# Optimization experiments

Hardware: AMD Instinct MI355X
Metric: run time of the kernel (lower is better)

## Reference

```python
import jax, jax.numpy as jnp
import numpy as np

N = 20000      # nodes
E = 640000     # edges (before self loops)
IN = 256       # in_channels == out_channels (forced by classifier size 4*in)
H1, C1 = 8, 16   # conv1: heads=8, out=16 -> concat 128
H2, C2 = 1, 256  # conv2: heads=1, out=out_channels
B = 4096       # article pairs
NEG_SLOPE = 0.2  # PyG GATv2Conv default negative_slope


def setup_inputs() -> dict:
    key = jax.random.key(0)
    ks = jax.random.split(key, 24)
    s = 0.05
    inp = {
        "gnn_x": jax.random.normal(ks[0], (N, IN), jnp.float32),
        "vanilla_x": jax.random.normal(ks[1], (N, IN), jnp.float32),
        "edge_src": jax.random.randint(ks[2], (E,), 0, N, jnp.int32),
        "edge_dst": jax.random.randint(ks[3], (E,), 0, N, jnp.int32),
        "a1_idx": jax.random.randint(ks[4], (B,), 0, N, jnp.int64),
        "a2_idx": jax.random.randint(ks[5], (B,), 0, N, jnp.int64),
        # conv1 params (lin_l, lin_r, att, bias)
        "Wl1": jax.random.normal(ks[6], (IN, H1 * C1), jnp.float32) * s,
        "bl1": jnp.zeros((H1 * C1,), jnp.float32),
        "Wr1": jax.random.normal(ks[7], (IN, H1 * C1), jnp.float32) * s,
        "br1": jnp.zeros((H1 * C1,), jnp.float32),
        "att1": jax.random.normal(ks[8], (H1, C1), jnp.float32) * s,
        "bias1": jnp.zeros((H1 * C1,), jnp.float32),
        # conv2 params
        "Wl2": jax.random.normal(ks[9], (H1 * C1, H2 * C2), jnp.float32) * s,
        "bl2": jnp.zeros((H2 * C2,), jnp.float32),
        "Wr2": jax.random.normal(ks[10], (H1 * C1, H2 * C2), jnp.float32) * s,
        "br2": jnp.zeros((H2 * C2,), jnp.float32),
        "att2": jax.random.normal(ks[11], (H2, C2), jnp.float32) * s,
        "bias2": jnp.zeros((H2 * C2,), jnp.float32),
        # classifier
        "Wc": jax.random.normal(ks[12], (4 * IN, 1), jnp.float32) * s,
        "bc": jnp.zeros((1,), jnp.float32),
    }
    return inp


def _gatv2_layer(x, src, dst, Wl, bl, Wr, br, att, bias):
    """GATv2Conv: x_l = lin_l(x)[src], x_r = lin_r(x)[dst];
    e = att . leaky_relu(x_l + x_r); segment softmax over dst; scatter-add x_l*alpha."""
    n = x.shape[0]
    h, c = att.shape
    xl = (x @ Wl + bl).reshape(n, h, c)
    xr = (x @ Wr + br).reshape(n, h, c)
    # per-edge attention logits [E, H]
    e = jnp.einsum('ehc,hc->eh', jax.nn.leaky_relu(xl[src] + xr[dst], NEG_SLOPE), att)
    # segment softmax over destination nodes (self loops guarantee non-empty segments)
    emax = jax.ops.segment_max(e, dst, num_segments=n)
    ex = jnp.exp(e - emax[dst])
    denom = jax.ops.segment_sum(ex, dst, num_segments=n)
    alpha = ex / denom[dst]                      # [E, H]
    out = jax.ops.segment_sum(alpha[:, :, None] * xl[src], dst, num_segments=n)  # [N,H,C]
    return out.reshape(n, h * c) + bias          # concat=True (heads=1 identical)


def reference(gnn_x, vanilla_x, Wl1, bl1, Wr1, br1, att1, bias1,
              Wl2, bl2, Wr2, br2, att2, bias2, Wc, bc,
              edge_src, edge_dst, a1_idx, a2_idx):
    n = gnn_x.shape[0]
    loops = jnp.arange(n, dtype=edge_src.dtype)
    src = jnp.concatenate([edge_src, loops])     # PyG add_self_loops=True
    dst = jnp.concatenate([edge_dst, loops])
    x = _gatv2_layer(gnn_x, src, dst, Wl1, bl1, Wr1, br1, att1, bias1)
    x = jax.nn.relu(x)
    x = _gatv2_layer(x, src, dst, Wl2, bl2, Wr2, br2, att2, bias2)
    combined = jnp.concatenate(
        [vanilla_x[a1_idx], vanilla_x[a2_idx], x[a1_idx], x[a2_idx]], axis=1)  # [B, 4*IN]
    logits = combined @ Wc + bc                  # [B, 1]
    return logits
```

## Files before the change

kernel.cpp:

```cpp
#include <hip/hip_runtime.h>
#include <math.h>

#define N_NODES 20000
#define M_PAD   20032
#define E_EDGES 640000
#define ET (E_EDGES + N_NODES)
#define IN_CH 256
#define D1 128
#define D2 256
#define BPAIRS 4096
#define NEG 0.2f
#define LOG2E 1.4426950408889634f

#define ZC_BLOCKS    20
#define WT_BLOCKS    32
#define XCONV_BLOCKS (M_PAD * IN_CH / 4 / 4 / 256)
#define RANK_BLOCKS  ((ET + 255) / 256)

#define G1X (M_PAD / 64)
#define G1Y (D1 / 64)
#define G1_BLOCKS (G1X * G1Y)
#define SCAT_BLOCKS ((ET + 255) / 256)

#if __has_builtin(__builtin_amdgcn_exp2f)
#define EXP2F(x) __builtin_amdgcn_exp2f(x)
#else
#define EXP2F(x) exp2f(x)
#endif

typedef __bf16 bf16x8 __attribute__((ext_vector_type(8)));
typedef float  f32x4  __attribute__((ext_vector_type(4)));
typedef float  f32x2  __attribute__((ext_vector_type(2)));
typedef unsigned short u16x4 __attribute__((ext_vector_type(4)));

__device__ __forceinline__ unsigned short f2b(float f) {
    unsigned int u = __float_as_uint(f);
    unsigned int r = u + 0x7FFFu + ((u >> 16) & 1u);
    return (unsigned short)(r >> 16);
}
__device__ __forceinline__ unsigned char f2f8(float f) {
    return (unsigned char)(__builtin_amdgcn_cvt_pk_fp8_f32(f, f, 0, false) & 0xFF);
}
template <bool HI>
__device__ __forceinline__ f32x2 f8up2(unsigned int u) {
    return __builtin_amdgcn_cvt_pk_f32_fp8((int)u, HI);
}
__device__ __forceinline__ f32x2 up2(unsigned int u) {
    f32x2 r;
    r.x = __uint_as_float(u << 16);
    r.y = __uint_as_float(u & 0xFFFF0000u);
    return r;
}
__device__ __forceinline__ f32x2 lrelu2(f32x2 s) {
    return __builtin_elementwise_max(s, s * NEG);
}
__device__ __forceinline__ float lrelu(float s) { return fmaxf(s, NEG * s); }

__device__ __forceinline__ void unpack8(uint4 u, float* v) {
    v[0] = __uint_as_float(u.x << 16); v[1] = __uint_as_float(u.x & 0xFFFF0000u);
    v[2] = __uint_as_float(u.y << 16); v[3] = __uint_as_float(u.y & 0xFFFF0000u);
    v[4] = __uint_as_float(u.z << 16); v[5] = __uint_as_float(u.z & 0xFFFF0000u);
    v[6] = __uint_as_float(u.w << 16); v[7] = __uint_as_float(u.w & 0xFFFF0000u);
}
__device__ __forceinline__ void unpack8_f8(uint2 u, float* v) {
    f32x2 a = f8up2<false>(u.x), b = f8up2<true>(u.x);
    f32x2 c = f8up2<false>(u.y), d = f8up2<true>(u.y);
    v[0] = a.x; v[1] = a.y; v[2] = b.x; v[3] = b.y;
    v[4] = c.x; v[5] = c.y; v[6] = d.x; v[7] = d.y;
}


__global__ __launch_bounds__(256) void prep_kernel(
        const float* __restrict__ gnn_x,
        const float* __restrict__ Wl1, const float* __restrict__ Wr1,
        const float* __restrict__ Wl2, const float* __restrict__ Wr2,
        unsigned short* __restrict__ xb,
        unsigned short* __restrict__ wt1l, unsigned short* __restrict__ wt1r,
        unsigned short* __restrict__ wt2l, unsigned short* __restrict__ wt2r,
        int* __restrict__ count) {
    __shared__ unsigned short tile[64 * 65];
    int bid = blockIdx.x;
    if (bid < ZC_BLOCKS) {
        int q = bid * 256 + threadIdx.x;
        if (q * 4 < N_NODES) {
            int4 z; z.x = z.y = z.z = z.w = 0;
            ((int4*)count)[q] = z;
        }
    } else if (bid < ZC_BLOCKS + WT_BLOCKS) {
        int t = bid - ZC_BLOCKS;
        int m = t >> 3;
        int tt = t & 7;
        const float* W;
        unsigned short* Wt;
        int K, N;
        if (m == 0)      { W = Wl1; Wt = wt1l; K = IN_CH; N = D1; }
        else if (m == 1) { W = Wr1; Wt = wt1r; K = IN_CH; N = D1; }
        else if (m == 2) { W = Wl2; Wt = wt2l; K = D1; N = D2; }
        else             { W = Wr2; Wt = wt2r; K = D1; N = D2; }
        int ntn = N >> 6;
        int k0 = (tt / ntn) << 6;
        int n0 = (tt % ntn) << 6;
        int c = threadIdx.x & 63;
        int rr = threadIdx.x >> 6;
#pragma unroll
        for (int ch = 0; ch < 16; ch++) {
            int row = rr * 16 + ch;
            tile[row * 65 + c] = f2b(W[(size_t)(k0 + row) * N + n0 + c]);
        }
        __syncthreads();
#pragma unroll
        for (int ch = 0; ch < 16; ch++) {
            int n = rr * 16 + ch;
            Wt[(size_t)(n0 + n) * K + k0 + c] = tile[c * 65 + n];
        }
    } else {
        int tid = (bid - ZC_BLOCKS - WT_BLOCKS) * 256 + threadIdx.x;
        const int NQ = M_PAD * IN_CH / 4;
        int q0 = tid * 4;
#pragma unroll
        for (int j = 0; j < 4; j++) {
            int qi = q0 + j;
            if (qi >= NQ) break;
            int e0 = qi * 4;
            int row = e0 >> 8;
            u16x4 o;
            if (row < N_NODES) {
                f32x4 v = __builtin_nontemporal_load((const f32x4*)(gnn_x + e0));
                o.x = f2b(v.x); o.y = f2b(v.y); o.z = f2b(v.z); o.w = f2b(v.w);
            } else {
                o.x = o.y = o.z = o.w = 0;
            }
            *(u16x4*)(xb + e0) = o;
        }
    }
}


__global__ __launch_bounds__(256) void rank_kernel(
        const int* __restrict__ edge_dst,
        int* __restrict__ count, int* __restrict__ rank) {
    int e = blockIdx.x * 256 + threadIdx.x;
    if (e >= ET) return;
    int dst = (e < E_EDGES) ? edge_dst[e] : (e - E_EDGES);
    rank[e] = atomicAdd(&count[dst], 1);
}


__global__ __launch_bounds__(1024) void scan_kernel(const int* __restrict__ count,
                                                    int* __restrict__ offsets) {
    const int PER = 20;
    int t = threadIdx.x;
    int base = t * PER;
    int local[PER];
    int sum = 0;
#pragma unroll
    for (int i = 0; i < PER; i++) {
        int idx = base + i;
        int v = (idx < N_NODES) ? count[idx] : 0;
        local[i] = sum;
        sum += v;
    }
    int lane = t & 63, wave = t >> 6;
    int s = sum;
#pragma unroll
    for (int off = 1; off < 64; off <<= 1) {
        int x = __shfl_up(s, off);
        if (lane >= off) s += x;
    }
    __shared__ int wsum[16];
    __shared__ int wpre[16];
    if (lane == 63) wsum[wave] = s;
    __syncthreads();
    if (t == 0) {
        int acc = 0;
        for (int w = 0; w < 16; w++) { wpre[w] = acc; acc += wsum[w]; }
        offsets[N_NODES] = acc;
    }
    __syncthreads();
    int thread_excl = wpre[wave] + (s - sum);
#pragma unroll
    for (int i = 0; i < PER; i++) {
        int idx = base + i;
        if (idx < N_NODES) offsets[idx] = thread_excl + local[i];
    }
}


template <int K>
__device__ __forceinline__ void dual_gemm_tile(
        const unsigned short* __restrict__ A,
        const unsigned short* __restrict__ Wtl,
        const unsigned short* __restrict__ Wtr,
        const float* __restrict__ bl, const float* __restrict__ br,
        unsigned char* __restrict__ Yl, unsigned short* __restrict__ Yr,
        int M, int NOUT, int bx, int by) {
    const int NK = K / 32;
    int wave = threadIdx.x >> 6;
    int lane = threadIdx.x & 63;
    int row0 = bx * 64;
    int col0 = (by * 4 + wave) * 16;
    int rsub = lane & 15;
    int koff = (lane >> 4) * 8;

    const unsigned short* ap  = A   + (size_t)(row0 + rsub) * K + koff;
    const unsigned short* bpl = Wtl + (size_t)(col0 + rsub) * K + koff;
    const unsigned short* bpr = Wtr + (size_t)(col0 + rsub) * K + koff;

    bf16x8 bfl[NK], bfr[NK];
#pragma unroll
    for (int kb = 0; kb < NK; kb++) {
        bfl[kb] = *(const bf16x8*)(bpl + kb * 32);
        bfr[kb] = *(const bf16x8*)(bpr + kb * 32);
    }

    f32x4 l0 = {0.f, 0.f, 0.f, 0.f};
    f32x4 l1 = l0, l2 = l0, l3 = l0, r0 = l0, r1 = l0, r2 = l0, r3 = l0;

#pragma unroll
    for (int kb = 0; kb < NK; kb++) {
        int off = kb * 32;
        bf16x8 a0 = *(const bf16x8*)(ap + off);
        bf16x8 a1 = *(const bf16x8*)(ap + 16 * K + off);
        bf16x8 a2 = *(const bf16x8*)(ap + 32 * K + off);
        bf16x8 a3 = *(const bf16x8*)(ap + 48 * K + off);
        l0 = __builtin_amdgcn_mfma_f32_16x16x32_bf16(a0, bfl[kb], l0, 0, 0, 0);
        r0 = __builtin_amdgcn_mfma_f32_16x16x32_bf16(a0, bfr[kb], r0, 0, 0, 0);
        l1 = __builtin_amdgcn_mfma_f32_16x16x32_bf16(a1, bfl[kb], l1, 0, 0, 0);
        r1 = __builtin_amdgcn_mfma_f32_16x16x32_bf16(a1, bfr[kb], r1, 0, 0, 0);
        l2 = __builtin_amdgcn_mfma_f32_16x16x32_bf16(a2, bfl[kb], l2, 0, 0, 0);
        r2 = __builtin_amdgcn_mfma_f32_16x16x32_bf16(a2, bfr[kb], r2, 0, 0, 0);
        l3 = __builtin_amdgcn_mfma_f32_16x16x32_bf16(a3, bfl[kb], l3, 0, 0, 0);
        r3 = __builtin_amdgcn_mfma_f32_16x16x32_bf16(a3, bfr[kb], r3, 0, 0, 0);
    }

    int colg = col0 + rsub;
    float bvl = bl[colg];
    float bvr = br[colg];
    int rbase = row0 + (lane >> 4) * 4;
#pragma unroll
    for (int t = 0; t < 4; t++) {
        f32x4 al = (t == 0) ? l0 : (t == 1) ? l1 : (t == 2) ? l2 : l3;
        f32x4 ar = (t == 0) ? r0 : (t == 1) ? r1 : (t == 2) ? r2 : r3;
#pragma unroll
        for (int r = 0; r < 4; r++) {
            int row = rbase + t * 16 + r;
            if (row < M) {
                Yl[(size_t)row * NOUT + colg] = f2f8(al[r] + bvl);
                Yr[(size_t)row * NOUT + colg] = f2b(ar[r] + bvr);
            }
        }
    }
}


__global__ __launch_bounds__(256) void gemm1_scatter_kernel(
        const unsigned short* __restrict__ A,
        const unsigned short* __restrict__ Wtl,
        const unsigned short* __restrict__ Wtr,
        const float* __restrict__ bl, const float* __restrict__ br,
        unsigned char* __restrict__ Yl, unsigned short* __restrict__ Yr,
        const int* __restrict__ edge_src, const int* __restrict__ edge_dst,
        const int* __restrict__ rank, const int* __restrict__ offsets,
        int* __restrict__ sorted_src) {
    int bid = blockIdx.x;
    if (bid < G1_BLOCKS) {
        dual_gemm_tile<IN_CH>(A, Wtl, Wtr, bl, br, Yl, Yr,
                              N_NODES, D1, bid % G1X, bid / G1X);
    } else {
        int e = (bid - G1_BLOCKS) * 256 + threadIdx.x;
        if (e >= ET) return;
        int dst = (e < E_EDGES) ? edge_dst[e] : (e - E_EDGES);
        int src = (e < E_EDGES) ? edge_src[e] : (e - E_EDGES);
        sorted_src[offsets[dst] + rank[e]] = src;
    }
}


template <int K>
__global__ __launch_bounds__(256) void dual_gemm_w32_kernel(
        const unsigned short* __restrict__ A,
        const unsigned short* __restrict__ Wtl,
        const unsigned short* __restrict__ Wtr,
        const float* __restrict__ bl, const float* __restrict__ br,
        unsigned char* __restrict__ Yl, unsigned short* __restrict__ Yr,
        int M, int NOUT) {
    const int NK = K / 32;
    int wave = threadIdx.x >> 6;
    int lane = threadIdx.x & 63;
    int row0 = blockIdx.x * 64;
    int col0 = blockIdx.y * 128 + wave * 32;
    int rsub = lane & 15;
    int koff = (lane >> 4) * 8;

    const unsigned short* ap = A + (size_t)(row0 + rsub) * K + koff;

    bf16x8 bfl[2][NK], bfr[2][NK];
#pragma unroll
    for (int c = 0; c < 2; c++) {
        const unsigned short* bpl = Wtl + (size_t)(col0 + c * 16 + rsub) * K + koff;
        const unsigned short* bpr = Wtr + (size_t)(col0 + c * 16 + rsub) * K + koff;
#pragma unroll
        for (int kb = 0; kb < NK; kb++) {
            bfl[c][kb] = *(const bf16x8*)(bpl + kb * 32);
            bfr[c][kb] = *(const bf16x8*)(bpr + kb * 32);
        }
    }

    f32x4 accl[2][4], accr[2][4];
#pragma unroll
    for (int c = 0; c < 2; c++)
#pragma unroll
        for (int t = 0; t < 4; t++) {
            accl[c][t] = (f32x4){0.f, 0.f, 0.f, 0.f};
            accr[c][t] = (f32x4){0.f, 0.f, 0.f, 0.f};
        }

#pragma unroll
    for (int kb = 0; kb < NK; kb++) {
        int off = kb * 32;
        bf16x8 a[4];
        a[0] = *(const bf16x8*)(ap + off);
        a[1] = *(const bf16x8*)(ap + 16 * K + off);
        a[2] = *(const bf16x8*)(ap + 32 * K + off);
        a[3] = *(const bf16x8*)(ap + 48 * K + off);
#pragma unroll
        for (int t = 0; t < 4; t++) {
#pragma unroll
            for (int c = 0; c < 2; c++) {
                accl[c][t] = __builtin_amdgcn_mfma_f32_16x16x32_bf16(
                    a[t], bfl[c][kb], accl[c][t], 0, 0, 0);
                accr[c][t] = __builtin_amdgcn_mfma_f32_16x16x32_bf16(
                    a[t], bfr[c][kb], accr[c][t], 0, 0, 0);
            }
        }
    }

    int rbase = row0 + (lane >> 4) * 4;
#pragma unroll
    for (int c = 0; c < 2; c++) {
        int colg = col0 + c * 16 + rsub;
        float bvl = bl[colg];
        float bvr = br[colg];
#pragma unroll
        for (int t = 0; t < 4; t++) {
#pragma unroll
            for (int r = 0; r < 4; r++) {
                int row = rbase + t * 16 + r;
                if (row < M) {
                    Yl[(size_t)row * NOUT + colg] = f2f8(accl[c][t][r] + bvl);
                    Yr[(size_t)row * NOUT + colg] = f2b(accr[c][t][r] + bvr);
                }
            }
        }
    }
}


__global__ __launch_bounds__(256) void aggregate1_kernel(
        const unsigned char* __restrict__ xl1, const unsigned short* __restrict__ xr1,
        const float* __restrict__ att1, const float* __restrict__ bias1,
        const int* __restrict__ offsets, const int* __restrict__ sorted_src,
        unsigned short* __restrict__ x1) {
    int wave = threadIdx.x >> 6;
    int lane = threadIdx.x & 63;
    int q = lane >> 4;
    int ql = lane & 15;
    int dst = blockIdx.x * 4 + wave;
    if (dst >= M_PAD) return;
    int c0 = ql * 8;
    if (dst >= N_NODES) {
        if (q == 0) {
            uint4 z; z.x = z.y = z.z = z.w = 0;
            *(uint4*)(x1 + (size_t)dst * D1 + c0) = z;
        }
        return;
    }

    uint4 xu = *(const uint4*)(xr1 + (size_t)dst * D1 + c0);
    f32x2 xr[4] = {up2(xu.x), up2(xu.y), up2(xu.z), up2(xu.w)};
    float4 aa0 = *(const float4*)(att1 + c0);
    float4 aa1 = *(const float4*)(att1 + c0 + 4);
    f32x2 att[4];
    att[0].x = aa0.x * LOG2E; att[0].y = aa0.y * LOG2E;
    att[1].x = aa0.z * LOG2E; att[1].y = aa0.w * LOG2E;
    att[2].x = aa1.x * LOG2E; att[2].y = aa1.y * LOG2E;
    att[3].x = aa1.z * LOG2E; att[3].y = aa1.w * LOG2E;

    int beg = offsets[dst], end = offsets[dst + 1];
    const unsigned char* base = xl1 + c0;

    float l = 0.f;
    f32x2 acc[4] = {{0.f,0.f},{0.f,0.f},{0.f,0.f},{0.f,0.f}};

    int i = beg;
    int s0 = sorted_src[min(i + q, end - 1)];
    uint2 g0 = *(const uint2*)(base + (size_t)s0 * D1);
    bool more1 = (i + 4) < end;
    uint2 g1;
    if (more1) {
        int s1 = sorted_src[min(i + 4 + q, end - 1)];
        g1 = *(const uint2*)(base + (size_t)s1 * D1);
    }
    while (true) {
        bool more2 = (i + 8) < end;
        uint2 g2;
        if (more2) {
            int s2 = sorted_src[min(i + 8 + q, end - 1)];
            g2 = *(const uint2*)(base + (size_t)s2 * D1);
        }
        bool act = (i + q) < end;
        f32x2 v0 = f8up2<false>(g0.x), v1 = f8up2<true>(g0.x);
        f32x2 v2 = f8up2<false>(g0.y), v3 = f8up2<true>(g0.y);
        f32x2 p2 = att[0] * lrelu2(v0 + xr[0]);
        p2 += att[1] * lrelu2(v1 + xr[1]);
        p2 += att[2] * lrelu2(v2 + xr[2]);
        p2 += att[3] * lrelu2(v3 + xr[3]);
        float p = p2.x + p2.y;
        p += __shfl_xor(p, 1);
        float w = act ? EXP2F(p) : 0.f;
        l += w;
        acc[0] += w * v0; acc[1] += w * v1; acc[2] += w * v2; acc[3] += w * v3;
        if (!more1) break;
        i += 4;
        g0 = g1; g1 = g2; more1 = more2;
    }
    l += __shfl_xor(l, 16);
    l += __shfl_xor(l, 32);
#pragma unroll
    for (int j = 0; j < 4; j++) {
        f32x2 t;
        t.x = __shfl_xor(acc[j].x, 16); t.y = __shfl_xor(acc[j].y, 16);
        acc[j] += t;
        t.x = __shfl_xor(acc[j].x, 32); t.y = __shfl_xor(acc[j].y, 32);
        acc[j] += t;
    }
    if (q == 0) {
        float inv = 1.f / l;
        float4 bb0 = *(const float4*)(bias1 + c0);
        float4 bb1 = *(const float4*)(bias1 + c0 + 4);
        unsigned short o[8];
        o[0] = f2b(fmaxf(acc[0].x * inv + bb0.x, 0.f));
        o[1] = f2b(fmaxf(acc[0].y * inv + bb0.y, 0.f));
        o[2] = f2b(fmaxf(acc[1].x * inv + bb0.z, 0.f));
        o[3] = f2b(fmaxf(acc[1].y * inv + bb0.w, 0.f));
        o[4] = f2b(fmaxf(acc[2].x * inv + bb1.x, 0.f));
        o[5] = f2b(fmaxf(acc[2].y * inv + bb1.y, 0.f));
        o[6] = f2b(fmaxf(acc[3].x * inv + bb1.z, 0.f));
        o[7] = f2b(fmaxf(acc[3].y * inv + bb1.w, 0.f));
        uint4 ov;
        ov.x = (unsigned int)o[0] | ((unsigned int)o[1] << 16);
        ov.y = (unsigned int)o[2] | ((unsigned int)o[3] << 16);
        ov.z = (unsigned int)o[4] | ((unsigned int)o[5] << 16);
        ov.w = (unsigned int)o[6] | ((unsigned int)o[7] << 16);
        *(uint4*)(x1 + (size_t)dst * D1 + c0) = ov;
    }
}


__global__ __launch_bounds__(256) void agg2_classifier_kernel(
        const unsigned char* __restrict__ xl2, const unsigned short* __restrict__ xr2,
        const float* __restrict__ att2, const float* __restrict__ bias2,
        const int* __restrict__ offsets, const int* __restrict__ sorted_src,
        const float* __restrict__ vanilla_x,
        const int* __restrict__ a1_raw, const int* __restrict__ a2_raw,
        const float* __restrict__ Wc, const float* __restrict__ bc,
        float* __restrict__ out) {
    __shared__ float x2row[2][D2];
    __shared__ float mrg[2][32][9];
    __shared__ float part[4];
    __shared__ int stride_s;
    int t = threadIdx.x;
    if (t < 64) {
        bool z = (t < 31) ? (a1_raw[1 + 2 * t] == 0) : true;
        unsigned long long m = __ballot(z);
        if (t == 0) stride_s = (m == ~0ull) ? 2 : 1;
    }
    __syncthreads();
    int stride = stride_s;
    int b = blockIdx.x;
    int a1 = a1_raw[(long)b * stride];
    int a2 = a2_raw[(long)b * stride];

    int wave = t >> 6;
    int d = wave >> 1;
    int ww = wave & 1;
    int lane = t & 63;
    int half = lane >> 5;
    int hl = lane & 31;
    int c0 = hl * 8;
    int dst = d ? a2 : a1;

    float xr[8], att[8];
    unpack8(*(const uint4*)(xr2 + (size_t)dst * D2 + c0), xr);
#pragma unroll
    for (int j = 0; j < 8; j++) att[j] = att2[c0 + j] * LOG2E;
    int beg = offsets[dst], end = offsets[dst + 1];
    const unsigned char* base = xl2 + c0;

    float l = 0.f;
    float acc[8];
#pragma unroll
    for (int j = 0; j < 8; j++) acc[j] = 0.f;

    int sub = 2 * ww + half;
    int i = beg;
    int s0 = sorted_src[min(i + sub, end - 1)];
    uint2 g0 = *(const uint2*)(base + (size_t)s0 * D2);
    bool more1 = (i + 4) < end;
    uint2 g1;
    if (more1) {
        int s1 = sorted_src[min(i + 4 + sub, end - 1)];
        g1 = *(const uint2*)(base + (size_t)s1 * D2);
    }
    while (true) {
        bool more2 = (i + 8) < end;
        uint2 g2;
        if (more2) {
            int s2 = sorted_src[min(i + 8 + sub, end - 1)];
            g2 = *(const uint2*)(base + (size_t)s2 * D2);
        }
        bool act = (i + sub) < end;
        float v[8];
        unpack8_f8(g0, v);
        float p = 0.f;
#pragma unroll
        for (int j = 0; j < 8; j++) p = fmaf(att[j], lrelu(v[j] + xr[j]), p);
        p += __shfl_xor(p, 1);
        p += __shfl_xor(p, 2);
        p += __shfl_xor(p, 4);
        p += __shfl_xor(p, 8);
        p += __shfl_xor(p, 16);
        float w = act ? EXP2F(p) : 0.f;
        l += w;
#pragma unroll
        for (int j = 0; j < 8; j++) acc[j] += w * v[j];
        if (!more1) break;
        i += 4;
        g0 = g1; g1 = g2; more1 = more2;
    }
    l += __shfl_xor(l, 32);
#pragma unroll
    for (int j = 0; j < 8; j++) acc[j] += __shfl_xor(acc[j], 32);
    if (ww == 1 && half == 0) {
        mrg[d][hl][0] = l;
#pragma unroll
        for (int j = 0; j < 8; j++) mrg[d][hl][1 + j] = acc[j];
    }
    __syncthreads();
    if (ww == 0 && half == 0) {
        l += mrg[d][hl][0];
#pragma unroll
        for (int j = 0; j < 8; j++) acc[j] += mrg[d][hl][1 + j];
        float inv = 1.f / l;
#pragma unroll
        for (int j = 0; j < 8; j++)
            x2row[d][c0 + j] = acc[j] * inv + bias2[c0 + j];
    }
    __syncthreads();

    float s = vanilla_x[(size_t)a1 * IN_CH + t] * Wc[t]
            + vanilla_x[(size_t)a2 * IN_CH + t] * Wc[IN_CH + t]
            + x2row[0][t] * Wc[2 * IN_CH + t]
            + x2row[1][t] * Wc[3 * IN_CH + t];
    s += __shfl_xor(s, 1);
    s += __shfl_xor(s, 2);
    s += __shfl_xor(s, 4);
    s += __shfl_xor(s, 8);
    s += __shfl_xor(s, 16);
    s += __shfl_xor(s, 32);
    if (lane == 0) part[wave] = s;
    __syncthreads();
    if (t == 0) out[b] = part[0] + part[1] + part[2] + part[3] + bc[0];
}


extern "C" void kernel_launch(void* const* d_in, const int* in_sizes, int n_in,
                              void* d_out, int out_size, void* d_ws, size_t ws_size,
                              hipStream_t stream) {
    const float* gnn_x     = (const float*)d_in[0];
    const float* vanilla_x = (const float*)d_in[1];
    const int*   edge_src  = (const int*)d_in[2];
    const int*   edge_dst  = (const int*)d_in[3];
    const int*   a1_idx    = (const int*)d_in[4];
    const int*   a2_idx    = (const int*)d_in[5];
    const float* Wl1   = (const float*)d_in[6];
    const float* bl1   = (const float*)d_in[7];
    const float* Wr1   = (const float*)d_in[8];
    const float* br1   = (const float*)d_in[9];
    const float* att1  = (const float*)d_in[10];
    const float* bias1 = (const float*)d_in[11];
    const float* Wl2   = (const float*)d_in[12];
    const float* bl2   = (const float*)d_in[13];
    const float* Wr2   = (const float*)d_in[14];
    const float* br2   = (const float*)d_in[15];
    const float* att2  = (const float*)d_in[16];
    const float* bias2 = (const float*)d_in[17];
    const float* Wc    = (const float*)d_in[18];
    const float* bc    = (const float*)d_in[19];
    float* out = (float*)d_out;

    char* p = (char*)d_ws;
    unsigned short* xb   = (unsigned short*)p; p += (size_t)M_PAD * IN_CH * 2;
    unsigned short* x1b  = (unsigned short*)p; p += (size_t)M_PAD * D1 * 2;
    unsigned char*  xl1b = (unsigned char*)p;  p += (size_t)N_NODES * D1;
    unsigned short* xr1b = (unsigned short*)p; p += (size_t)N_NODES * D1 * 2;
    unsigned char*  xl2b = (unsigned char*)p;  p += (size_t)N_NODES * D2;
    unsigned short* xr2b = (unsigned short*)p; p += (size_t)N_NODES * D2 * 2;
    unsigned short* wt1l = (unsigned short*)p; p += (size_t)D1 * IN_CH * 2;
    unsigned short* wt1r = (unsigned short*)p; p += (size_t)D1 * IN_CH * 2;
    unsigned short* wt2l = (unsigned short*)p; p += (size_t)D2 * D1 * 2;
    unsigned short* wt2r = (unsigned short*)p; p += (size_t)D2 * D1 * 2;
    int* count      = (int*)p; p += (size_t)N_NODES * 4;
    int* offsets    = (int*)p; p += (size_t)(N_NODES + 4) * 4;
    int* rank       = (int*)p; p += (size_t)ET * 4;
    int* sorted_src = (int*)p; p += (size_t)ET * 4;

    prep_kernel<<<ZC_BLOCKS + WT_BLOCKS + XCONV_BLOCKS, 256, 0, stream>>>(
        gnn_x, Wl1, Wr1, Wl2, Wr2,
        xb, wt1l, wt1r, wt2l, wt2r, count);

    rank_kernel<<<RANK_BLOCKS, 256, 0, stream>>>(edge_dst, count, rank);

    scan_kernel<<<1, 1024, 0, stream>>>(count, offsets);

    gemm1_scatter_kernel<<<G1_BLOCKS + SCAT_BLOCKS, 256, 0, stream>>>(
        xb, wt1l, wt1r, bl1, br1, xl1b, xr1b,
        edge_src, edge_dst, rank, offsets, sorted_src);

    aggregate1_kernel<<<M_PAD / 4, 256, 0, stream>>>(
        xl1b, xr1b, att1, bias1, offsets, sorted_src, x1b);

    dim3 g2(M_PAD / 64, D2 / 128);
    dual_gemm_w32_kernel<D1><<<g2, 256, 0, stream>>>(
        x1b, wt2l, wt2r, bl2, br2, xl2b, xr2b, N_NODES, D2);

    agg2_classifier_kernel<<<BPAIRS, 256, 0, stream>>>(
        xl2b, xr2b, att2, bias2, offsets, sorted_src,
        vanilla_x, a1_idx, a2_idx, Wc, bc, out);
}
```

Baseline: 261.6 us.

## Fuse rank counting and scan into prep kernel with last-block scan

Merges the edge rank atomics, the weight transpose and the input bf16 conversion into a single front kernel. The exclusive scan over per-node counts now runs inside whichever rank block finishes last, detected with a done counter plus threadfence. A small zero kernel clears the counts and the done flag up front. This cuts two kernel launches and their serialization gaps. In exchange the scan runs on only 256 threads of one block, with serial per-thread loops that re-read count, and it relies on a correct threadfence/atomic pattern.

```diff
diff --git a/kernel.cpp b/kernel.cpp
--- a/kernel.cpp
+++ b/kernel.cpp
@@ -12,10 +12,11 @@
 #define NEG 0.2f
 #define LOG2E 1.4426950408889634f
 
-#define ZC_BLOCKS    20
-#define WT_BLOCKS    32
+#define ZERO_BLOCKS 20
+#define WT_BLOCKS   32
 #define XCONV_BLOCKS (M_PAD * IN_CH / 4 / 4 / 256)
 #define RANK_BLOCKS  ((ET + 255) / 256)
+#define FRONT_BLOCKS (RANK_BLOCKS + WT_BLOCKS + XCONV_BLOCKS)
 
 #define G1X (M_PAD / 64)
 #define G1Y (D1 / 64)
@@ -70,24 +71,84 @@
 }
 
 
-__global__ __launch_bounds__(256) void prep_kernel(
+__global__ __launch_bounds__(256) void zero_kernel(int* __restrict__ count) {
+    int q = blockIdx.x * 256 + threadIdx.x;
+    int4 z; z.x = z.y = z.z = z.w = 0;
+    ((int4*)count)[q] = z;
+}
+
+__device__ __forceinline__ void scan256(const int* __restrict__ count,
+                                        int* __restrict__ offsets,
+                                        int* wbuf) {
+    const int PER = 79;
+    int t = threadIdx.x;
+    int base = t * PER;
+    int sum = 0;
+#pragma unroll 8
+    for (int i = 0; i < PER; i++) {
+        int idx = base + i;
+        if (idx < N_NODES) sum += count[idx];
+    }
+    int lane = t & 63, wave = t >> 6;
+    int s = sum;
+#pragma unroll
+    for (int off = 1; off < 64; off <<= 1) {
+        int x = __shfl_up(s, off);
+        if (lane >= off) s += x;
+    }
+    int* wsum = wbuf;
+    int* wpre = wbuf + 4;
+    if (lane == 63) wsum[wave] = s;
+    __syncthreads();
+    if (t == 0) {
+        int acc = 0;
+        for (int w = 0; w < 4; w++) { wpre[w] = acc; acc += wsum[w]; }
+    }
+    __syncthreads();
+    int excl = wpre[wave] + (s - sum);
+    if (t == 255) offsets[N_NODES] = excl + sum;
+    int run = excl;
+#pragma unroll 8
+    for (int i = 0; i < PER; i++) {
+        int idx = base + i;
+        if (idx < N_NODES) { offsets[idx] = run; run += count[idx]; }
+    }
+}
+
+
+__global__ __launch_bounds__(256) void front_kernel(
         const float* __restrict__ gnn_x,
         const float* __restrict__ Wl1, const float* __restrict__ Wr1,
         const float* __restrict__ Wl2, const float* __restrict__ Wr2,
+        const int* __restrict__ edge_dst,
         unsigned short* __restrict__ xb,
         unsigned short* __restrict__ wt1l, unsigned short* __restrict__ wt1r,
         unsigned short* __restrict__ wt2l, unsigned short* __restrict__ wt2r,
-        int* __restrict__ count) {
-    __shared__ unsigned short tile[64 * 65];
+        int* __restrict__ count, int* __restrict__ done,
+        int* __restrict__ rank, int* __restrict__ offsets) {
+    __shared__ __align__(16) char smem[8448];
     int bid = blockIdx.x;
-    if (bid < ZC_BLOCKS) {
-        int q = bid * 256 + threadIdx.x;
-        if (q * 4 < N_NODES) {
-            int4 z; z.x = z.y = z.z = z.w = 0;
-            ((int4*)count)[q] = z;
-        }
-    } else if (bid < ZC_BLOCKS + WT_BLOCKS) {
-        int t = bid - ZC_BLOCKS;
+    int tid = threadIdx.x;
+    if (bid < RANK_BLOCKS) {
+        int e = bid * 256 + tid;
+        if (e < ET) {
+            int dst = (e < E_EDGES) ? edge_dst[e] : (e - E_EDGES);
+            rank[e] = atomicAdd(&count[dst], 1);
+        }
+        __shared__ int islast;
+        if (tid == 0) {
+            __threadfence();
+            int old = atomicAdd(done, 1);
+            islast = (old == RANK_BLOCKS - 1) ? 1 : 0;
+        }
+        __syncthreads();
+        if (islast) {
+            __threadfence();
+            scan256(count, offsets, (int*)smem);
+        }
+    } else if (bid < RANK_BLOCKS + WT_BLOCKS) {
+        unsigned short* tile = (unsigned short*)smem;
+        int t = bid - RANK_BLOCKS;
         int m = t >> 3;
         int tt = t & 7;
         const float* W;
@@ -100,8 +161,8 @@
         int ntn = N >> 6;
         int k0 = (tt / ntn) << 6;
         int n0 = (tt % ntn) << 6;
-        int c = threadIdx.x & 63;
-        int rr = threadIdx.x >> 6;
+        int c = tid & 63;
+        int rr = tid >> 6;
 #pragma unroll
         for (int ch = 0; ch < 16; ch++) {
             int row = rr * 16 + ch;
@@ -114,9 +175,9 @@
             Wt[(size_t)(n0 + n) * K + k0 + c] = tile[c * 65 + n];
         }
     } else {
-        int tid = (bid - ZC_BLOCKS - WT_BLOCKS) * 256 + threadIdx.x;
+        int t = (bid - RANK_BLOCKS - WT_BLOCKS) * 256 + tid;
         const int NQ = M_PAD * IN_CH / 4;
-        int q0 = tid * 4;
+        int q0 = t * 4;
 #pragma unroll
         for (int j = 0; j < 4; j++) {
             int qi = q0 + j;
@@ -132,56 +193,6 @@
             }
             *(u16x4*)(xb + e0) = o;
         }
-    }
-}
-
-
-__global__ __launch_bounds__(256) void rank_kernel(
-        const int* __restrict__ edge_dst,
-        int* __restrict__ count, int* __restrict__ rank) {
-    int e = blockIdx.x * 256 + threadIdx.x;
-    if (e >= ET) return;
-    int dst = (e < E_EDGES) ? edge_dst[e] : (e - E_EDGES);
-    rank[e] = atomicAdd(&count[dst], 1);
-}
-
-
-__global__ __launch_bounds__(1024) void scan_kernel(const int* __restrict__ count,
-                                                    int* __restrict__ offsets) {
-    const int PER = 20;
-    int t = threadIdx.x;
-    int base = t * PER;
-    int local[PER];
-    int sum = 0;
-#pragma unroll
-    for (int i = 0; i < PER; i++) {
-        int idx = base + i;
-        int v = (idx < N_NODES) ? count[idx] : 0;
-        local[i] = sum;
-        sum += v;
-    }
-    int lane = t & 63, wave = t >> 6;
-    int s = sum;
-#pragma unroll
-    for (int off = 1; off < 64; off <<= 1) {
-        int x = __shfl_up(s, off);
-        if (lane >= off) s += x;
-    }
-    __shared__ int wsum[16];
-    __shared__ int wpre[16];
-    if (lane == 63) wsum[wave] = s;
-    __syncthreads();
-    if (t == 0) {
-        int acc = 0;
-        for (int w = 0; w < 16; w++) { wpre[w] = acc; acc += wsum[w]; }
-        offsets[N_NODES] = acc;
-    }
-    __syncthreads();
-    int thread_excl = wpre[wave] + (s - sum);
-#pragma unroll
-    for (int i = 0; i < PER; i++) {
-        int idx = base + i;
-        if (idx < N_NODES) offsets[idx] = thread_excl + local[i];
     }
 }
 
@@ -610,18 +621,17 @@
     unsigned short* wt1r = (unsigned short*)p; p += (size_t)D1 * IN_CH * 2;
     unsigned short* wt2l = (unsigned short*)p; p += (size_t)D2 * D1 * 2;
     unsigned short* wt2r = (unsigned short*)p; p += (size_t)D2 * D1 * 2;
-    int* count      = (int*)p; p += (size_t)N_NODES * 4;
+    int* count      = (int*)p; p += (size_t)20480 * 4;
     int* offsets    = (int*)p; p += (size_t)(N_NODES + 4) * 4;
     int* rank       = (int*)p; p += (size_t)ET * 4;
     int* sorted_src = (int*)p; p += (size_t)ET * 4;
-
-    prep_kernel<<<ZC_BLOCKS + WT_BLOCKS + XCONV_BLOCKS, 256, 0, stream>>>(
-        gnn_x, Wl1, Wr1, Wl2, Wr2,
-        xb, wt1l, wt1r, wt2l, wt2r, count);
-
-    rank_kernel<<<RANK_BLOCKS, 256, 0, stream>>>(edge_dst, count, rank);
-
-    scan_kernel<<<1, 1024, 0, stream>>>(count, offsets);
+    int* done = count + 20032;
+
+    zero_kernel<<<ZERO_BLOCKS, 256, 0, stream>>>(count);
+
+    front_kernel<<<FRONT_BLOCKS, 256, 0, stream>>>(
+        gnn_x, Wl1, Wr1, Wl2, Wr2, edge_dst,
+        xb, wt1l, wt1r, wt2l, wt2r, count, done, rank, offsets);
 
     gemm1_scatter_kernel<<<G1_BLOCKS + SCAT_BLOCKS, 256, 0, stream>>>(
         xb, wt1l, wt1r, bl1, br1, xl1b, xr1b,
```

New measurement: 352.3 us. 1.35x slower.
